# Kernel optimization log

Hardware: AMD Instinct MI355X
Metric: run time of the kernel (lower is better)

Reference implementation:

```python
import jax, jax.numpy as jnp
import numpy as np

B, S, D, H = 4, 2048, 512, 8
HD = D // H  # head_dim = 64


def setup_inputs() -> dict:
    key = jax.random.key(0)
    ks = jax.random.split(key, 16)
    sd = 1.0 / np.sqrt(D)
    def lin(ka, kb):
        W = jax.random.uniform(ka, (D, D), jnp.float32, -sd, sd)
        b = jax.random.uniform(kb, (D,), jnp.float32, -sd, sd)
        return W, b
    Wq, bq = lin(ks[0], ks[1])
    Wk, bk = lin(ks[2], ks[3])
    Wv, bv = lin(ks[4], ks[5])
    Wo, bo = lin(ks[6], ks[7])
    Ws, bs = lin(ks[8], ks[9])
    Wsh, bsh = lin(ks[10], ks[11])
    mod1_feat = jax.random.normal(ks[12], (B, S, D), jnp.float32)
    mod2_feat = jax.random.normal(ks[13], (B, S, D), jnp.float32)
    return {"mod1_feat": mod1_feat, "mod2_feat": mod2_feat,
            "Wq": Wq, "bq": bq, "Wk": Wk, "bk": bk, "Wv": Wv, "bv": bv,
            "Wo": Wo, "bo": bo, "Ws": Ws, "bs": bs, "Wsh": Wsh, "bsh": bsh}


def _heads(x):
    # [B, S, D] -> [B, H, S, HD]
    b, s, _ = x.shape
    return x.reshape(b, s, H, HD).transpose(0, 2, 1, 3)


def reference(mod1_feat, mod2_feat, Wq, bq, Wk, bk, Wv, bv, Wo, bo, Ws, bs, Wsh, bsh):
    Q = _heads(mod1_feat @ Wq + bq)
    K = _heads(mod2_feat @ Wk + bk)
    V = _heads(mod2_feat @ Wv + bv)
    scale = _heads(mod2_feat @ Ws + bs)
    shift = _heads(mod2_feat @ Wsh + bsh)
    K = K * scale + shift
    V = V * scale + shift
    scores = jnp.einsum('bhqd,bhkd->bhqk', Q, K) / jnp.sqrt(jnp.float32(HD))
    attn = jax.nn.softmax(scores, axis=-1)
    out = jnp.einsum('bhqk,bhkd->bhqd', attn, V)  # [B, H, S, HD]
    out = out.transpose(0, 2, 1, 3).reshape(mod1_feat.shape[0], -1, H * HD)
    return out @ Wo + bo
```

## Files before the change

### kernel.cpp

```cpp
#include <hip/hip_runtime.h>
#include <hip/hip_bf16.h>
#include <cstdint>
#include <cstddef>

typedef __bf16 bf16_t;
typedef __bf16 bf16x8 __attribute__((ext_vector_type(8)));
typedef __bf16 bf16x4 __attribute__((ext_vector_type(4)));
typedef float f32x4 __attribute__((ext_vector_type(4)));

#define DEVINL static __device__ __forceinline__

constexpr int B_ = 4, S_ = 2048, D_ = 512, H_ = 8, HD_ = 64;
constexpr int M_ = B_ * S_;
constexpr int NIN = 14;

DEVINL bf16x8 load8g(const bf16_t* p) { return *reinterpret_cast<const bf16x8*>(p); }

DEVINL int swcol(int col, int row) {
  return (col & ~63) | ((((col >> 3) ^ row) & 7) << 3) | (col & 7);
}

DEVINL int pK(int row) { return (row & 3) | (((row >> 3) & 1) << 2); }
DEVINL int swcolK(int col, int row) {
  return (col & ~63) | ((((col >> 3) ^ pK(row)) & 7) << 3) | (col & 7);
}

DEVINL void gl2lds(const bf16_t* g, bf16_t* l) {
  __builtin_amdgcn_global_load_lds(
      (const __attribute__((address_space(1))) void*)g,
      (__attribute__((address_space(3))) void*)l, 16, 0, 0);
}

DEVINL void stage16(bf16_t* dst, const void* src, size_t off, bool f32) {
  if (f32) {
    const float* p = (const float*)src + off;
    bf16x8 v0, v1;
#pragma unroll
    for (int j = 0; j < 8; ++j) { v0[j] = (bf16_t)p[j]; v1[j] = (bf16_t)p[8 + j]; }
    *reinterpret_cast<bf16x8*>(dst)     = v0;
    *reinterpret_cast<bf16x8*>(dst + 8) = v1;
  } else {
    const bf16_t* p = (const bf16_t*)src + off;
    *reinterpret_cast<bf16x8*>(dst)     = load8g(p);
    *reinterpret_cast<bf16x8*>(dst + 8) = load8g(p + 8);
  }
}

DEVINL float readf(const void* p, size_t i, bool f32) {
  return f32 ? ((const float*)p)[i] : (float)((const bf16_t*)p)[i];
}

struct DetectArgs { const uint16_t* p[NIN]; int n[NIN]; int* flags; };

__global__ __launch_bounds__(64) void detect_kernel(DetectArgs a) {
  const int z = blockIdx.x;
  const uint16_t* p = a.p[z];
  const int n = a.n[z];
  const int t = threadIdx.x;
  int cnt = 0;
  for (int i = t; i < n; i += 64) {
    const int e = (p[i] >> 7) & 0xFF;
    cnt += (e >= 200);
  }
#pragma unroll
  for (int off = 32; off > 0; off >>= 1) cnt += __shfl_down(cnt, off, 64);
  if (t == 0) a.flags[z] = (cnt > 16) ? 1 : 0;
}

struct CvtArgs { const void* src[2]; bf16_t* dst[2]; int idx[2]; const int* flags; };

__global__ __launch_bounds__(256) void cvt_kernel(CvtArgs a) {
  const int z = blockIdx.y;
  const bool f32 = a.flags[a.idx[z]] != 0;
  const size_t i = ((size_t)blockIdx.x * 256 + threadIdx.x) * 8;
  const int row = (int)(i >> 9);
  const int col = (int)(i & 511);
  bf16_t* dst = a.dst[z] + (size_t)row * 512 + swcol(col, row);
  if (f32) {
    const float* p = (const float*)a.src[z] + i;
    bf16x8 v;
#pragma unroll
    for (int j = 0; j < 8; ++j) v[j] = (bf16_t)p[j];
    *reinterpret_cast<bf16x8*>(dst) = v;
  } else {
    *reinterpret_cast<bf16x8*>(dst) = load8g((const bf16_t*)a.src[z] + i);
  }
}

struct TransArgs { const void* src[6]; int srcIdx[6]; bf16_t* dst[6]; const int* flags; };

__global__ __launch_bounds__(256) void transpose_kernel(TransArgs a) {
  __shared__ bf16_t tile[64][80];
  const int w = blockIdx.z;
  const void* src = a.src[w];
  const bool f32 = a.flags[a.srcIdx[w]] != 0;
  bf16_t* dst = a.dst[w];
  const int k0 = blockIdx.x * 64, n0 = blockIdx.y * 64;
  const int t = threadIdx.x;
  const int r = t >> 2, c0 = (t & 3) * 16;
  stage16(&tile[r][c0], src, (size_t)(k0 + r) * 512 + n0 + c0, f32);
  __syncthreads();
  const int orow = n0 + r;
  bf16_t* o = dst + (size_t)orow * 512;
#pragma unroll
  for (int half = 0; half < 2; ++half) {
    bf16x8 ov;
#pragma unroll
    for (int j = 0; j < 8; ++j) ov[j] = tile[c0 + half * 8 + j][r];
    *reinterpret_cast<bf16x8*>(o + swcol(k0 + c0 + half * 8, orow)) = ov;
  }
}

struct GemmBatch {
  const bf16_t* A[3];
  const bf16_t* Bt[3];
  const void* bias[3]; int bIdx[3];
  void* C[3];          int cIdx[3];
  const int* flags;
};

__global__ __launch_bounds__(256) void gemm_bt_kernel(GemmBatch args) {
  constexpr int K = 512, N = 512;
  __shared__ bf16_t As[2][128][64];
  __shared__ bf16_t Bs[2][64][64];
  const int z = blockIdx.z;
  const bf16_t* Ag  = args.A[z];
  const bf16_t* Btg = args.Bt[z];
  const void* biag  = args.bias[z];
  void* Cg          = args.C[z];
  const bool bf32 = args.bIdx[z] >= 0 && args.flags[args.bIdx[z]];
  const bool cf32 = args.cIdx[z] >= 0 && args.flags[args.cIdx[z]];
  const int m0 = blockIdx.x * 128, n0 = blockIdx.y * 64;
  const int t = threadIdx.x, lane = t & 63, wave = t >> 6;
  const int l16 = lane & 15, quad = lane >> 4;
  const int wm = wave * 32;
  const int lr = lane >> 3, lc = (lane & 7) * 8;

  auto stage = [&](int buf, int k0) {
#pragma unroll
    for (int s = 0; s < 4; ++s) {
      const int r = wm + s * 8;
      gl2lds(Ag + (size_t)(m0 + r + lr) * K + k0 + lc, &As[buf][r][0]);
    }
#pragma unroll
    for (int s = 0; s < 2; ++s) {
      const int r = wave * 16 + s * 8;
      gl2lds(Btg + (size_t)(n0 + r + lr) * K + k0 + lc, &Bs[buf][r][0]);
    }
  };

  f32x4 acc[2][4] = {};
  stage(0, 0);

  for (int kt = 0; kt < K / 64; ++kt) {
    const int cur = kt & 1;
    __syncthreads();
    if (kt + 1 < K / 64) stage(1 - cur, (kt + 1) * 64);
#pragma unroll
    for (int ks = 0; ks < 2; ++ks) {
      const int sw = swcol(ks * 32 + quad * 8, l16);
      bf16x8 af[2], bfr[4];
#pragma unroll
      for (int i = 0; i < 2; ++i)
        af[i] = *reinterpret_cast<const bf16x8*>(&As[cur][wm + i * 16 + l16][sw]);
#pragma unroll
      for (int j = 0; j < 4; ++j)
        bfr[j] = *reinterpret_cast<const bf16x8*>(&Bs[cur][j * 16 + l16][sw]);
#pragma unroll
      for (int i = 0; i < 2; ++i)
#pragma unroll
        for (int j = 0; j < 4; ++j)
          acc[i][j] = __builtin_amdgcn_mfma_f32_16x16x32_bf16(af[i], bfr[j], acc[i][j], 0, 0, 0);
    }
  }
#pragma unroll
  for (int j = 0; j < 4; ++j) {
    const int col = n0 + j * 16 + l16;
    const float bv = readf(biag, col, bf32);
#pragma unroll
    for (int i = 0; i < 2; ++i) {
      const int rowb = m0 + wm + i * 16 + quad * 4;
#pragma unroll
      for (int r = 0; r < 4; ++r) {
        const size_t idx = (size_t)(rowb + r) * N + col;
        const float v = acc[i][j][r] + bv;
        if (cf32) ((float*)Cg)[idx] = v;
        else      ((bf16_t*)Cg)[idx] = (bf16_t)v;
      }
    }
  }
}

struct GemmModArgs {
  const bf16_t* A;
  const bf16_t* Bt[2];
  const void* bias[2]; int bIdx[2];
  const bf16_t* Sc;
  const bf16_t* Sh;
  bf16_t* Kmod;
  bf16_t* VtT;
  const int* flags;
};

__global__ __launch_bounds__(256) void gemm_mod_kernel(GemmModArgs args) {
  constexpr int K = 512;
  __shared__ bf16_t As[2][128][64];
  __shared__ bf16_t Bs[2][64][64];
  const int z = blockIdx.z;
  const bf16_t* Ag  = args.A;
  const bf16_t* Btg = args.Bt[z];
  const void* biag  = args.bias[z];
  const bool bf32 = args.bIdx[z] >= 0 && args.flags[args.bIdx[z]];
  const int m0 = blockIdx.x * 128, n0 = blockIdx.y * 64;
  const int t = threadIdx.x, lane = t & 63, wave = t >> 6;
  const int l16 = lane & 15, quad = lane >> 4;
  const int wm = wave * 32;
  const int lr = lane >> 3, lc = (lane & 7) * 8;

  auto stage = [&](int buf, int k0) {
#pragma unroll
    for (int s = 0; s < 4; ++s) {
      const int r = wm + s * 8;
      gl2lds(Ag + (size_t)(m0 + r + lr) * K + k0 + lc, &As[buf][r][0]);
    }
#pragma unroll
    for (int s = 0; s < 2; ++s) {
      const int r = wave * 16 + s * 8;
      gl2lds(Btg + (size_t)(n0 + r + lr) * K + k0 + lc, &Bs[buf][r][0]);
    }
  };

  f32x4 acc[2][4] = {};
  stage(0, 0);

  for (int kt = 0; kt < K / 64; ++kt) {
    const int cur = kt & 1;
    __syncthreads();
    if (kt + 1 < K / 64) stage(1 - cur, (kt + 1) * 64);
#pragma unroll
    for (int ks = 0; ks < 2; ++ks) {
      const int sw = swcol(ks * 32 + quad * 8, l16);
      bf16x8 af[2], bfr[4];
#pragma unroll
      for (int i = 0; i < 2; ++i)
        af[i] = *reinterpret_cast<const bf16x8*>(&As[cur][wm + i * 16 + l16][sw]);
#pragma unroll
      for (int j = 0; j < 4; ++j)
        bfr[j] = *reinterpret_cast<const bf16x8*>(&Bs[cur][j * 16 + l16][sw]);
#pragma unroll
      for (int i = 0; i < 2; ++i)
#pragma unroll
        for (int j = 0; j < 4; ++j)
          acc[i][j] = __builtin_amdgcn_mfma_f32_16x16x32_bf16(af[i], bfr[j], acc[i][j], 0, 0, 0);
    }
  }
#pragma unroll
  for (int j = 0; j < 4; ++j) {
    const int col = n0 + j * 16 + l16;
    const float bv = readf(biag, col, bf32);
#pragma unroll
    for (int i = 0; i < 2; ++i) {
      const int rowb = m0 + wm + i * 16 + quad * 4;
      if (z == 0) {
#pragma unroll
        for (int r = 0; r < 4; ++r) {
          const int row = rowb + r;
          const size_t idx = (size_t)row * 512 + col;
          const float sc = (float)args.Sc[idx], sh = (float)args.Sh[idx];
          args.Kmod[(size_t)row * 512 + swcolK(col, row)] = (bf16_t)fmaf(acc[i][j][r] + bv, sc, sh);
        }
      } else {
        bf16x4 pack;
#pragma unroll
        for (int r = 0; r < 4; ++r) {
          const size_t idx = (size_t)(rowb + r) * 512 + col;
          const float sc = (float)args.Sc[idx], sh = (float)args.Sh[idx];
          pack[r] = (bf16_t)fmaf(acc[i][j][r] + bv, sc, sh);
        }
        const int bb = rowb >> 11;
        const int ss = rowb & 2047;
        const int hh = col >> 6, dd = col & 63;
        *reinterpret_cast<bf16x4*>(
            args.VtT + (((size_t)(bb * H_ + hh)) * HD_ + dd) * S_ + swcol(ss, dd)) = pack;
      }
    }
  }
}

__global__ __launch_bounds__(256) void attn_kernel(const bf16_t* Q, const bf16_t* Kb,
                                                   const bf16_t* Vt, bf16_t* O) {
  __shared__ bf16_t Ks[2][64][64];
  __shared__ bf16_t Vs[2][64][64];
  const int i = blockIdx.x;
  const int xcd = i & 7, g = i >> 3;
  const int slice = xcd * 4 + (g & 3);
  const int qt = g >> 2;
  const int b = slice >> 3, h = slice & 7;
  const int t = threadIdx.x, wave = t >> 6, lane = t & 63;
  const int l16 = lane & 15, quad = lane >> 4;
  const int q0 = qt * 64 + wave * 16;
  const int lr = lane >> 3, lc = (lane & 7) * 8;

  bf16x8 ones;
#pragma unroll
  for (int j = 0; j < 8; ++j) ones[j] = (bf16_t)1.0f;

  bf16x8 qf[2];
  {
    const size_t qrow = ((size_t)b * S_ + q0 + l16) * D_ + h * HD_;
    qf[0] = load8g(Q + qrow + quad * 8);
    qf[1] = load8g(Q + qrow + 32 + quad * 8);
  }

  f32x4 oacc[4] = {};
  f32x4 lacc = {};

  const size_t kbase = (size_t)b * S_ * D_ + h * HD_;
  const size_t vbase = ((size_t)(b * H_ + h)) * HD_ * S_;

  const int rbase = ((l16 >> 2) << 3) | (l16 & 3);
  int koff[2][4];
#pragma unroll
  for (int j = 0; j < 4; ++j) {
    const int rho = rbase + (j >> 1) * 32 + (j & 1) * 4;
#pragma unroll
    for (int dc = 0; dc < 2; ++dc)
      koff[dc][j] = rho * 64 + swcolK(dc * 32 + quad * 8, rho);
  }
  const int voff[2] = { swcol(quad * 8, l16), swcol(32 + quad * 8, l16) };

  auto stage = [&](int buf, int k0) {
#pragma unroll
    for (int s = 0; s < 2; ++s) {
      const int r = wave * 16 + s * 8;
      gl2lds(Kb + kbase + (size_t)(k0 + r + lr) * D_ + lc, &Ks[buf][r][0]);
      gl2lds(Vt + vbase + (size_t)(r + lr) * S_ + k0 + lc, &Vs[buf][r][0]);
    }
  };

  stage(0, 0);

  constexpr float CE = 0.18033688011112042f;

  for (int kt = 0; kt < S_ / 64; ++kt) {
    const int cur = kt & 1;
    __syncthreads();
    if (kt + 1 < S_ / 64) stage(1 - cur, (kt + 1) * 64);
    f32x4 sacc[4] = {};
    const bf16_t* ksbase = &Ks[cur][0][0];
#pragma unroll
    for (int dc = 0; dc < 2; ++dc) {
      bf16x8 kf[4];
#pragma unroll
      for (int j = 0; j < 4; ++j)
        kf[j] = *reinterpret_cast<const bf16x8*>(ksbase + koff[dc][j]);
#pragma unroll
      for (int j = 0; j < 4; ++j)
        sacc[j] = __builtin_amdgcn_mfma_f32_16x16x32_bf16(kf[j], qf[dc], sacc[j], 0, 0, 0);
    }
#pragma unroll
    for (int kc = 0; kc < 2; ++kc) {
      bf16x8 vf[4];
#pragma unroll
      for (int dj = 0; dj < 4; ++dj)
        vf[dj] = *reinterpret_cast<const bf16x8*>(&Vs[cur][dj * 16 + l16][voff[kc]]);
      bf16x8 bp;
#pragma unroll
      for (int r = 0; r < 4; ++r) {
        bp[r]     = (bf16_t)__builtin_amdgcn_exp2f(fminf(sacc[kc * 2][r]     * CE, 57.5f));
        bp[4 + r] = (bf16_t)__builtin_amdgcn_exp2f(fminf(sacc[kc * 2 + 1][r] * CE, 57.5f));
      }
#pragma unroll
      for (int dj = 0; dj < 4; ++dj)
        oacc[dj] = __builtin_amdgcn_mfma_f32_16x16x32_bf16(vf[dj], bp, oacc[dj], 0, 0, 0);
      lacc = __builtin_amdgcn_mfma_f32_16x16x32_bf16(ones, bp, lacc, 0, 0, 0);
    }
  }
  {
    const float linv = 1.0f / fmaxf(lacc[0], 1e-30f);
    const int q = q0 + l16;
    const size_t orow = ((size_t)b * S_ + q) * D_ + h * HD_;
#pragma unroll
    for (int dj = 0; dj < 4; ++dj) {
      bf16x4 pack;
#pragma unroll
      for (int r = 0; r < 4; ++r) pack[r] = (bf16_t)(oacc[dj][r] * linv);
      *reinterpret_cast<bf16x4*>(&O[orow + swcol(dj * 16 + quad * 4, q)]) = pack;
    }
  }
}

extern "C" void kernel_launch(void* const* d_in, const int* in_sizes, int n_in,
                              void* d_out, int out_size, void* d_ws, size_t ws_size,
                              hipStream_t stream) {
  (void)n_in; (void)out_size; (void)ws_size;

  char* ws = (char*)d_ws;
  auto alloc = [&](size_t bytes) -> char* {
    char* p = ws; ws += (bytes + 255) & ~(size_t)255; return p;
  };
  int* flags = (int*)alloc(64 * sizeof(int));
  const size_t wbytes = (size_t)512 * 512 * sizeof(bf16_t);
  const size_t fbytes = (size_t)M_ * D_ * sizeof(bf16_t);
  bf16_t* wt    = (bf16_t*)alloc(6 * wbytes);
  bf16_t* m1b   = (bf16_t*)alloc(fbytes);
  bf16_t* m2b   = (bf16_t*)alloc(fbytes);
  bf16_t* q_buf = (bf16_t*)alloc(fbytes);
  bf16_t* stmp  = (bf16_t*)alloc(fbytes);
  bf16_t* shtmp = (bf16_t*)alloc(fbytes);
  bf16_t* kmod  = (bf16_t*)alloc(fbytes);
  bf16_t* vtb    = m1b;
  bf16_t* attn_b = stmp;

  bf16_t* wtq  = wt + 0 * 512 * 512;
  bf16_t* wtk  = wt + 1 * 512 * 512;
  bf16_t* wtv  = wt + 2 * 512 * 512;
  bf16_t* wts  = wt + 3 * 512 * 512;
  bf16_t* wtsh = wt + 4 * 512 * 512;
  bf16_t* wto  = wt + 5 * 512 * 512;

  DetectArgs da;
  for (int i = 0; i < NIN; ++i) {
    da.p[i] = (const uint16_t*)d_in[i];
    da.n[i] = in_sizes[i] < 2048 ? in_sizes[i] : 2048;
  }
  da.flags = flags;
  hipLaunchKernelGGL(detect_kernel, dim3(NIN), dim3(64), 0, stream, da);

  CvtArgs ca;
  ca.src[0] = d_in[0]; ca.dst[0] = m1b; ca.idx[0] = 0;
  ca.src[1] = d_in[1]; ca.dst[1] = m2b; ca.idx[1] = 1;
  ca.flags = flags;
  hipLaunchKernelGGL(cvt_kernel, dim3(M_ * D_ / 2048, 2), dim3(256), 0, stream, ca);

  TransArgs ta;
  const int widx[6] = {2, 4, 6, 10, 12, 8};
  bf16_t* wdst[6] = {wtq, wtk, wtv, wts, wtsh, wto};
  for (int i = 0; i < 6; ++i) { ta.src[i] = d_in[widx[i]]; ta.srcIdx[i] = widx[i]; ta.dst[i] = wdst[i]; }
  ta.flags = flags;
  hipLaunchKernelGGL(transpose_kernel, dim3(8, 8, 6), dim3(256), 0, stream, ta);

  GemmBatch g1;
  g1.A[0] = m1b; g1.A[1] = m2b; g1.A[2] = m2b;
  g1.Bt[0] = wtq; g1.Bt[1] = wts; g1.Bt[2] = wtsh;
  g1.bias[0] = d_in[3];  g1.bIdx[0] = 3;
  g1.bias[1] = d_in[11]; g1.bIdx[1] = 11;
  g1.bias[2] = d_in[13]; g1.bIdx[2] = 13;
  g1.C[0] = q_buf; g1.cIdx[0] = -1;
  g1.C[1] = stmp;  g1.cIdx[1] = -1;
  g1.C[2] = shtmp; g1.cIdx[2] = -1;
  g1.flags = flags;
  hipLaunchKernelGGL(gemm_bt_kernel, dim3(M_ / 128, 8, 3), dim3(256), 0, stream, g1);

  GemmModArgs gm;
  gm.A = m2b;
  gm.Bt[0] = wtk; gm.Bt[1] = wtv;
  gm.bias[0] = d_in[5]; gm.bIdx[0] = 5;
  gm.bias[1] = d_in[7]; gm.bIdx[1] = 7;
  gm.Sc = stmp; gm.Sh = shtmp;
  gm.Kmod = kmod; gm.VtT = vtb;
  gm.flags = flags;
  hipLaunchKernelGGL(gemm_mod_kernel, dim3(M_ / 128, 8, 2), dim3(256), 0, stream, gm);

  hipLaunchKernelGGL(attn_kernel, dim3(1024), dim3(256), 0, stream,
                     q_buf, kmod, vtb, attn_b);

  GemmBatch g2;
  for (int i = 0; i < 3; ++i) {
    g2.A[i] = attn_b;
    g2.Bt[i] = wto;
    g2.bias[i] = d_in[9]; g2.bIdx[i] = 9;
    g2.C[i] = d_out; g2.cIdx[i] = 0;
  }
  g2.flags = flags;
  hipLaunchKernelGGL(gemm_bt_kernel, dim3(M_ / 128, 8, 1), dim3(256), 0, stream, g2);
}
```

Measured before the change: 226.5 us.

## Use 8-wave attention blocks with triple-buffered K/V prefetch

The attention kernel now launches 512-thread blocks covering 128 queries each, halving the block count and sharing each K/V tile across twice as many waves. Staging becomes a three-slot ring with two tiles in flight, and explicit vmcnt waits plus barriers replace the per-iteration __syncthreads. The goal is to cut redundant K/V global loads and hide load latency better. The costs are more LDS per block and fewer blocks to fill the GPU. Block-to-slice mapping still uses the old formula; with 512 blocks, qt = g>>2 spans 0..15, which at 128 rows per tile covers all 2048 queries.

```diff
diff --git a/kernel.cpp b/kernel.cpp
--- a/kernel.cpp
+++ b/kernel.cpp
@@ -287,10 +287,10 @@
   }
 }
 
-__global__ __launch_bounds__(256) void attn_kernel(const bf16_t* Q, const bf16_t* Kb,
+__global__ __launch_bounds__(512) void attn_kernel(const bf16_t* Q, const bf16_t* Kb,
                                                    const bf16_t* Vt, bf16_t* O) {
-  __shared__ bf16_t Ks[2][64][64];
-  __shared__ bf16_t Vs[2][64][64];
+  __shared__ bf16_t Ks[3][64][64];
+  __shared__ bf16_t Vs[3][64][64];
   const int i = blockIdx.x;
   const int xcd = i & 7, g = i >> 3;
   const int slice = xcd * 4 + (g & 3);
@@ -298,7 +298,7 @@
   const int b = slice >> 3, h = slice & 7;
   const int t = threadIdx.x, wave = t >> 6, lane = t & 63;
   const int l16 = lane & 15, quad = lane >> 4;
-  const int q0 = qt * 64 + wave * 16;
+  const int q0 = qt * 128 + wave * 16;
   const int lr = lane >> 3, lc = (lane & 7) * 8;
 
   bf16x8 ones;
@@ -329,23 +329,15 @@
   }
   const int voff[2] = { swcol(quad * 8, l16), swcol(32 + quad * 8, l16) };
 
-  auto stage = [&](int buf, int k0) {
-#pragma unroll
-    for (int s = 0; s < 2; ++s) {
-      const int r = wave * 16 + s * 8;
-      gl2lds(Kb + kbase + (size_t)(k0 + r + lr) * D_ + lc, &Ks[buf][r][0]);
-      gl2lds(Vt + vbase + (size_t)(r + lr) * S_ + k0 + lc, &Vs[buf][r][0]);
-    }
+  auto stage = [&](int slot, int k0) {
+    const int r = wave * 8;
+    gl2lds(Kb + kbase + (size_t)(k0 + r + lr) * D_ + lc, &Ks[slot][r][0]);
+    gl2lds(Vt + vbase + (size_t)(r + lr) * S_ + k0 + lc, &Vs[slot][r][0]);
   };
 
-  stage(0, 0);
-
   constexpr float CE = 0.18033688011112042f;
 
-  for (int kt = 0; kt < S_ / 64; ++kt) {
-    const int cur = kt & 1;
-    __syncthreads();
-    if (kt + 1 < S_ / 64) stage(1 - cur, (kt + 1) * 64);
+  auto compute = [&](int cur) {
     f32x4 sacc[4] = {};
     const bf16_t* ksbase = &Ks[cur][0][0];
 #pragma unroll
@@ -375,7 +367,27 @@
         oacc[dj] = __builtin_amdgcn_mfma_f32_16x16x32_bf16(vf[dj], bp, oacc[dj], 0, 0, 0);
       lacc = __builtin_amdgcn_mfma_f32_16x16x32_bf16(ones, bp, lacc, 0, 0, 0);
     }
-  }
+  };
+
+  stage(0, 0);
+  stage(1, 64);
+
+  constexpr int NT = S_ / 64;
+  int cur = 0;
+  for (int kt = 0; kt < NT - 1; ++kt) {
+    asm volatile("s_waitcnt vmcnt(2)\n\ts_barrier" ::: "memory");
+    __builtin_amdgcn_sched_barrier(0);
+    if (kt + 2 < NT) {
+      const int slot2 = cur == 0 ? 2 : cur - 1;
+      stage(slot2, (kt + 2) * 64);
+    }
+    compute(cur);
+    cur = (cur == 2) ? 0 : cur + 1;
+  }
+  asm volatile("s_waitcnt vmcnt(0)\n\ts_barrier" ::: "memory");
+  __builtin_amdgcn_sched_barrier(0);
+  compute(cur);
+
   {
     const float linv = 1.0f / fmaxf(lacc[0], 1e-30f);
     const int q = q0 + l16;
@@ -462,7 +474,7 @@
   gm.flags = flags;
   hipLaunchKernelGGL(gemm_mod_kernel, dim3(M_ / 128, 8, 2), dim3(256), 0, stream, gm);
 
-  hipLaunchKernelGGL(attn_kernel, dim3(1024), dim3(256), 0, stream,
+  hipLaunchKernelGGL(attn_kernel, dim3(512), dim3(512), 0, stream,
                      q_buf, kmod, vtb, attn_b);
 
   GemmBatch g2;
```

Result: faster. 214.1 us (-5.5%).
